# Kernel tuning notes

Measured on AMD Instinct MI355X. Metric: run time of the kernel, lower is better.

## Reference

```python
import jax, jax.numpy as jnp
import numpy as np

P = 31998
VOCAB = P + 2        # 32000
EMBED = 1024
HIDDEN = 2048
NUM_LAYERS = 4
BATCH = 64
SEQ = 512


def setup_inputs() -> dict:
    key = jax.random.key(0)
    ks = jax.random.split(key, 7)
    X = jax.random.randint(ks[0], (BATCH, SEQ), 0, VOCAB, dtype=jnp.int64 if jax.config.jax_enable_x64 else jnp.int32)
    emb = jax.random.normal(ks[1], (VOCAB, EMBED), dtype=jnp.float32)
    W_xh = jax.random.normal(ks[2], (EMBED, HIDDEN), dtype=jnp.float32)
    W_hh = jax.random.normal(ks[3], (HIDDEN, HIDDEN), dtype=jnp.float32)
    W_hy = jax.random.normal(ks[4], (HIDDEN, VOCAB), dtype=jnp.float32)
    b_h = jnp.zeros((HIDDEN,), dtype=jnp.float32)
    b_y = jnp.zeros((VOCAB,), dtype=jnp.float32)
    return {"X": X, "emb": emb, "W_xh": W_xh, "W_hh": W_hh, "W_hy": W_hy, "b_h": b_h, "b_y": b_y}


def reference(X, emb, W_xh, W_hh, W_hy, b_h, b_y):
    # Original torch code re-initializes new_h from x_t each timestep (no state
    # carried across t), so every timestep is independent and only the last
    # timestep feeds the output. Vectorize over all timesteps faithfully.
    x = emb[X]                                   # [B, T, E]
    h = jnp.tanh(jnp.einsum('bte,eh->bth', x, W_xh) + b_h)   # [B, T, H]
    for _ in range(NUM_LAYERS):
        h = jnp.tanh(jnp.einsum('bth,hk->btk', h, W_hh) + b_h)
    out = h[:, -1, :] @ W_hy + b_y               # [B, VOCAB]  (last timestep only)
    return out
```

## Files before the change

### kernel.cpp

```cpp
#include <hip/hip_runtime.h>
#include <hip/hip_bf16.h>

#define BATCH 64
#define SEQT  512
#define EMB   1024
#define HID   2048
#define VOC   32000
#define KSPLIT 8

using bf16x8 = __attribute__((ext_vector_type(8))) __bf16;
using f32x4  = __attribute__((ext_vector_type(4))) float;

__device__ __forceinline__ void split2(float x, __bf16& hi, __bf16& lo) {
  hi = (__bf16)x;
  lo = (__bf16)(x - (float)hi);
}

template <int KTOT, bool GATHER, bool PACKOUT>
__global__ __launch_bounds__(1024) void layer_kernel(
    const int* __restrict__ X, const float* __restrict__ emb,
    const __hip_bfloat16* __restrict__ hin_hi,
    const __hip_bfloat16* __restrict__ hin_lo,
    const float* __restrict__ W, const float* __restrict__ bias,
    __hip_bfloat16* __restrict__ hout_hi,
    __hip_bfloat16* __restrict__ hout_lo,
    unsigned* __restrict__ hp, float* __restrict__ hf) {
  constexpr int KCHUNK = KTOT / 16;
  constexpr int KSTEPS = KCHUNK / 32;
  __shared__ float red[16 * 16 * 40];

  const int tid = threadIdx.x;
  const int w = tid >> 6;
  const int l = tid & 63;
  const int ln = l & 15;
  const int lg = l >> 4;
  const int n0 = (blockIdx.x & 127) * 16;
  const int mb = (blockIdx.x >> 7) * 32;

  f32x4 acc[2];
#pragma unroll
  for (int mt = 0; mt < 2; ++mt) acc[mt] = f32x4{0.f, 0.f, 0.f, 0.f};

  const float* grow[2];
#pragma unroll
  for (int mt = 0; mt < 2; ++mt) {
    if constexpr (GATHER) {
      const int m = mb + ln + 16 * mt;
      const int tok = X[m * SEQT + (SEQT - 1)];
      grow[mt] = emb + (size_t)tok * EMB;
    } else {
      grow[mt] = nullptr;
    }
  }

  const int kwave = w * KCHUNK + lg * 8;
  const float* Wc = W + n0 + ln;

  float wv[KSTEPS * 8];
#pragma unroll
  for (int j = 0; j < KSTEPS * 8; ++j)
    wv[j] = Wc[(size_t)(kwave + (j >> 3) * 32 + (j & 7)) * HID];

  bf16x8 Ah[2][KSTEPS], Al[2][KSTEPS];
  if constexpr (GATHER) {
#pragma unroll
    for (int mt = 0; mt < 2; ++mt)
#pragma unroll
      for (int ks = 0; ks < KSTEPS; ++ks) {
        const float* p = grow[mt] + kwave + ks * 32;
        const f32x4 v0 = *reinterpret_cast<const f32x4*>(p);
        const f32x4 v1 = *reinterpret_cast<const f32x4*>(p + 4);
#pragma unroll
        for (int i = 0; i < 4; ++i) {
          __bf16 h_, l_;
          split2(v0[i], h_, l_);
          Ah[mt][ks][i] = h_;
          Al[mt][ks][i] = l_;
          split2(v1[i], h_, l_);
          Ah[mt][ks][4 + i] = h_;
          Al[mt][ks][4 + i] = l_;
        }
      }
  } else {
#pragma unroll
    for (int mt = 0; mt < 2; ++mt)
#pragma unroll
      for (int ks = 0; ks < KSTEPS; ++ks) {
        const size_t off = (size_t)(mb + ln + 16 * mt) * KTOT + kwave + ks * 32;
        Ah[mt][ks] = *reinterpret_cast<const bf16x8*>(hin_hi + off);
        Al[mt][ks] = *reinterpret_cast<const bf16x8*>(hin_lo + off);
      }
  }

#pragma unroll
  for (int ks = 0; ks < KSTEPS; ++ks) {
    bf16x8 bhi, blo;
#pragma unroll
    for (int i = 0; i < 8; ++i) {
      __bf16 h_, l_;
      split2(wv[ks * 8 + i], h_, l_);
      bhi[i] = h_;
      blo[i] = l_;
    }
#pragma unroll
    for (int mt = 0; mt < 2; ++mt) {
      acc[mt] = __builtin_amdgcn_mfma_f32_16x16x32_bf16(Ah[mt][ks], bhi, acc[mt], 0, 0, 0);
      acc[mt] = __builtin_amdgcn_mfma_f32_16x16x32_bf16(Al[mt][ks], bhi, acc[mt], 0, 0, 0);
      acc[mt] = __builtin_amdgcn_mfma_f32_16x16x32_bf16(Ah[mt][ks], blo, acc[mt], 0, 0, 0);
    }
  }

  float* dst = &red[(w * 16 + ln) * 40 + lg * 4];
#pragma unroll
  for (int mt = 0; mt < 2; ++mt)
    *reinterpret_cast<f32x4*>(dst + mt * 16) = acc[mt];

  __syncthreads();

  if (tid < 512) {
    const int m = tid >> 4, n = tid & 15;
    float s = 0.f;
#pragma unroll
    for (int ww = 0; ww < 16; ++ww) s += red[(ww * 16 + n) * 40 + m];
    s += bias[n0 + n];
    const float hval = tanhf(s);
    if constexpr (PACKOUT) {
      const int c = n0 + n;
      const int mg = mb + m;
      hf[(size_t)c * 64 + mg] = hval;
      const float partner = __shfl_xor(hval, 1, 64);
      if ((tid & 1) == 0) {
        using fp2 = __attribute__((ext_vector_type(2))) __fp16;
        const fp2 pk = __builtin_amdgcn_cvt_pkrtz(hval, partner);
        hp[(size_t)(c >> 1) * 64 + mg] = __builtin_bit_cast(unsigned, pk);
      }
    } else {
      __bf16 h_, l_;
      split2(hval, h_, l_);
      const size_t off = (size_t)(mb + m) * HID + (n0 + n);
      hout_hi[off] = *reinterpret_cast<__hip_bfloat16*>(&h_);
      hout_lo[off] = *reinterpret_cast<__hip_bfloat16*>(&l_);
    }
  }
}

__global__ __launch_bounds__(256) void out_mfma(
    const __hip_bfloat16* __restrict__ hhi, const float* __restrict__ Why,
    float* __restrict__ scratch) {
  __shared__ float lds[2 * 32 * 128];

  const int tid = threadIdx.x;
  const int w = tid >> 6;
  const int l = tid & 63;
  const int ln = l & 15;
  const int lg = l >> 4;
  const int nt = blockIdx.x % 250;
  const int kq = blockIdx.x / 250;
  const int n0 = nt * 128;
  const int k0 = kq * 256;

  const int srow = tid >> 5;
  const int scol = (tid & 31) * 4;

  f32x4 acc[4][2];
#pragma unroll
  for (int mf = 0; mf < 4; ++mf)
#pragma unroll
    for (int nf = 0; nf < 2; ++nf) acc[mf][nf] = f32x4{0.f, 0.f, 0.f, 0.f};

  f32x4 st[4];

#define GLOAD(ks_)                                                           \
  {                                                                          \
    _Pragma("unroll") for (int i = 0; i < 4; ++i) {                          \
      st[i] = __builtin_nontemporal_load(reinterpret_cast<const f32x4*>(     \
          Why + (size_t)(k0 + (ks_) * 32 + srow + i * 8) * VOC + n0 + scol));\
    }                                                                        \
  }

#define DSWRITE(buf_)                                                        \
  {                                                                          \
    float* lb_ = lds + (buf_) * (32 * 128);                                  \
    _Pragma("unroll") for (int i = 0; i < 4; ++i) {                          \
      *reinterpret_cast<f32x4*>(lb_ + (srow + i * 8) * 128 + scol) = st[i];  \
    }                                                                        \
  }

#define COMPUTE(buf_, ks_)                                                   \
  {                                                                          \
    const float* lb_ = lds + (buf_) * (32 * 128);                            \
    bf16x8 a_[4];                                                            \
    _Pragma("unroll") for (int mf = 0; mf < 4; ++mf) {                       \
      a_[mf] = *reinterpret_cast<const bf16x8*>(                             \
          hhi + (size_t)(mf * 16 + ln) * HID + k0 + (ks_) * 32 + lg * 8);    \
    }                                                                        \
    bf16x8 b_[2];                                                            \
    _Pragma("unroll") for (int nf = 0; nf < 2; ++nf) {                       \
      _Pragma("unroll") for (int i = 0; i < 8; ++i) {                        \
        b_[nf][i] =                                                          \
            (__bf16)lb_[(lg * 8 + i) * 128 + w * 32 + nf * 16 + ln];         \
      }                                                                      \
    }                                                                        \
    _Pragma("unroll") for (int mf = 0; mf < 4; ++mf) {                       \
      _Pragma("unroll") for (int nf = 0; nf < 2; ++nf) {                     \
        acc[mf][nf] = __builtin_amdgcn_mfma_f32_16x16x32_bf16(               \
            a_[mf], b_[nf], acc[mf][nf], 0, 0, 0);                           \
      }                                                                      \
    }                                                                        \
  }

  GLOAD(0);
  DSWRITE(0);
  __syncthreads();

#pragma unroll
  for (int ks = 0; ks < 8; ++ks) {
    if (ks < 7) GLOAD(ks + 1);
    COMPUTE(ks & 1, ks);
    __syncthreads();
    if (ks < 7) {
      DSWRITE((ks + 1) & 1);
      __syncthreads();
    }
  }
#undef COMPUTE
#undef DSWRITE
#undef GLOAD

  float* sc = scratch + (size_t)kq * ((size_t)BATCH * VOC);
#pragma unroll
  for (int mf = 0; mf < 4; ++mf) {
#pragma unroll
    for (int nf = 0; nf < 2; ++nf) {
#pragma unroll
      for (int j = 0; j < 4; ++j) {
        const int row = mf * 16 + lg * 4 + j;
        const int col = n0 + w * 32 + nf * 16 + ln;
        sc[(size_t)row * VOC + col] = acc[mf][nf][j];
      }
    }
  }
}

__global__ __launch_bounds__(256) void reduce_out(
    const float* __restrict__ scratch, const float* __restrict__ by,
    float* __restrict__ out) {
  const int n = blockIdx.x * 256 + threadIdx.x;
  const int m = blockIdx.y;
  float s = by[n];
#pragma unroll
  for (int q = 0; q < KSPLIT; ++q)
    s += scratch[(size_t)q * ((size_t)BATCH * VOC) + (size_t)m * VOC + n];
  __builtin_nontemporal_store(s, out + (size_t)m * VOC + n);
}

extern "C" void kernel_launch(void* const* d_in, const int* in_sizes, int n_in,
                              void* d_out, int out_size, void* d_ws,
                              size_t ws_size, hipStream_t stream) {
  const int* X = (const int*)d_in[0];
  const float* emb = (const float*)d_in[1];
  const float* W_xh = (const float*)d_in[2];
  const float* W_hh = (const float*)d_in[3];
  const float* W_hy = (const float*)d_in[4];
  const float* b_h = (const float*)d_in[5];
  const float* b_y = (const float*)d_in[6];
  float* out = (float*)d_out;

  char* ws = (char*)d_ws;
  const size_t PLANE = (size_t)BATCH * HID;
  __hip_bfloat16* hA_hi = (__hip_bfloat16*)ws;
  __hip_bfloat16* hA_lo = hA_hi + PLANE;
  __hip_bfloat16* hB_hi = hA_lo + PLANE;
  __hip_bfloat16* hB_lo = hB_hi + PLANE;
  float* scratch = (float*)(ws + 4 * PLANE * sizeof(__hip_bfloat16));

  dim3 blk(1024), grd(256);
  layer_kernel<EMB, true, false><<<grd, blk, 0, stream>>>(
      X, emb, nullptr, nullptr, W_xh, b_h, hA_hi, hA_lo, nullptr, nullptr);
  layer_kernel<HID, false, false><<<grd, blk, 0, stream>>>(
      nullptr, nullptr, hA_hi, hA_lo, W_hh, b_h, hB_hi, hB_lo, nullptr, nullptr);
  layer_kernel<HID, false, false><<<grd, blk, 0, stream>>>(
      nullptr, nullptr, hB_hi, hB_lo, W_hh, b_h, hA_hi, hA_lo, nullptr, nullptr);
  layer_kernel<HID, false, false><<<grd, blk, 0, stream>>>(
      nullptr, nullptr, hA_hi, hA_lo, W_hh, b_h, hB_hi, hB_lo, nullptr, nullptr);
  layer_kernel<HID, false, false><<<grd, blk, 0, stream>>>(
      nullptr, nullptr, hB_hi, hB_lo, W_hh, b_h, hA_hi, hA_lo, nullptr, nullptr);

  out_mfma<<<dim3(2000), dim3(256), 0, stream>>>(hA_hi, W_hy, scratch);
  reduce_out<<<dim3(125, 64), dim3(256), 0, stream>>>(scratch, b_y, out);
}
```

Before: 136.6 us.

## Halve output GEMM k-split and use triple-buffered LDS pipeline with single barrier

The output projection now splits K into 4 chunks of 512 instead of 8 of 256, so 1000 blocks each run 16 k-steps and the reduce kernel sums fewer partial planes. The LDS staging moves from double to triple buffering with two register staging sets, which lets global loads run two steps ahead and drops one __syncthreads per step. The unused PACKOUT path is removed from the layer kernel. The trade-offs are fewer blocks in flight, more LDS and register use per block, and a longer serial loop per block.

Measured after the change: 126.3 us. 7.5% less time.

```diff
diff --git a/kernel.cpp b/kernel.cpp
--- a/kernel.cpp
+++ b/kernel.cpp
@@ -6,7 +6,7 @@
 #define EMB   1024
 #define HID   2048
 #define VOC   32000
-#define KSPLIT 8
+#define KSPLIT 4
 
 using bf16x8 = __attribute__((ext_vector_type(8))) __bf16;
 using f32x4  = __attribute__((ext_vector_type(4))) float;
@@ -16,15 +16,14 @@
   lo = (__bf16)(x - (float)hi);
 }
 
-template <int KTOT, bool GATHER, bool PACKOUT>
+template <int KTOT, bool GATHER>
 __global__ __launch_bounds__(1024) void layer_kernel(
     const int* __restrict__ X, const float* __restrict__ emb,
     const __hip_bfloat16* __restrict__ hin_hi,
     const __hip_bfloat16* __restrict__ hin_lo,
     const float* __restrict__ W, const float* __restrict__ bias,
     __hip_bfloat16* __restrict__ hout_hi,
-    __hip_bfloat16* __restrict__ hout_lo,
-    unsigned* __restrict__ hp, float* __restrict__ hf) {
+    __hip_bfloat16* __restrict__ hout_lo) {
   constexpr int KCHUNK = KTOT / 16;
   constexpr int KSTEPS = KCHUNK / 32;
   __shared__ float red[16 * 16 * 40];
@@ -124,30 +123,18 @@
     for (int ww = 0; ww < 16; ++ww) s += red[(ww * 16 + n) * 40 + m];
     s += bias[n0 + n];
     const float hval = tanhf(s);
-    if constexpr (PACKOUT) {
-      const int c = n0 + n;
-      const int mg = mb + m;
-      hf[(size_t)c * 64 + mg] = hval;
-      const float partner = __shfl_xor(hval, 1, 64);
-      if ((tid & 1) == 0) {
-        using fp2 = __attribute__((ext_vector_type(2))) __fp16;
-        const fp2 pk = __builtin_amdgcn_cvt_pkrtz(hval, partner);
-        hp[(size_t)(c >> 1) * 64 + mg] = __builtin_bit_cast(unsigned, pk);
-      }
-    } else {
-      __bf16 h_, l_;
-      split2(hval, h_, l_);
-      const size_t off = (size_t)(mb + m) * HID + (n0 + n);
-      hout_hi[off] = *reinterpret_cast<__hip_bfloat16*>(&h_);
-      hout_lo[off] = *reinterpret_cast<__hip_bfloat16*>(&l_);
-    }
+    __bf16 h_, l_;
+    split2(hval, h_, l_);
+    const size_t off = (size_t)(mb + m) * HID + (n0 + n);
+    hout_hi[off] = *reinterpret_cast<__hip_bfloat16*>(&h_);
+    hout_lo[off] = *reinterpret_cast<__hip_bfloat16*>(&l_);
   }
 }
 
 __global__ __launch_bounds__(256) void out_mfma(
     const __hip_bfloat16* __restrict__ hhi, const float* __restrict__ Why,
     float* __restrict__ scratch) {
-  __shared__ float lds[2 * 32 * 128];
+  __shared__ float lds[3 * 32 * 128];
 
   const int tid = threadIdx.x;
   const int w = tid >> 6;
@@ -157,7 +144,8 @@
   const int nt = blockIdx.x % 250;
   const int kq = blockIdx.x / 250;
   const int n0 = nt * 128;
-  const int k0 = kq * 256;
+  const int k0 = kq * 512;
+  constexpr int NS = 16;
 
   const int srow = tid >> 5;
   const int scol = (tid & 31) * 4;
@@ -168,21 +156,21 @@
 #pragma unroll
     for (int nf = 0; nf < 2; ++nf) acc[mf][nf] = f32x4{0.f, 0.f, 0.f, 0.f};
 
-  f32x4 st[4];
-
-#define GLOAD(ks_)                                                           \
+  f32x4 stA[4], stB[4];
+
+#define GLOAD(ks_, st_)                                                      \
   {                                                                          \
     _Pragma("unroll") for (int i = 0; i < 4; ++i) {                          \
-      st[i] = __builtin_nontemporal_load(reinterpret_cast<const f32x4*>(     \
+      st_[i] = __builtin_nontemporal_load(reinterpret_cast<const f32x4*>(    \
           Why + (size_t)(k0 + (ks_) * 32 + srow + i * 8) * VOC + n0 + scol));\
     }                                                                        \
   }
 
-#define DSWRITE(buf_)                                                        \
+#define DSWRITE(buf_, st_)                                                   \
   {                                                                          \
     float* lb_ = lds + (buf_) * (32 * 128);                                  \
     _Pragma("unroll") for (int i = 0; i < 4; ++i) {                          \
-      *reinterpret_cast<f32x4*>(lb_ + (srow + i * 8) * 128 + scol) = st[i];  \
+      *reinterpret_cast<f32x4*>(lb_ + (srow + i * 8) * 128 + scol) = st_[i]; \
     }                                                                        \
   }
 
@@ -209,19 +197,22 @@
     }                                                                        \
   }
 
-  GLOAD(0);
-  DSWRITE(0);
+  GLOAD(0, stA);
+  DSWRITE(0, stA);
+  GLOAD(1, stB);
   __syncthreads();
 
 #pragma unroll
-  for (int ks = 0; ks < 8; ++ks) {
-    if (ks < 7) GLOAD(ks + 1);
-    COMPUTE(ks & 1, ks);
-    __syncthreads();
-    if (ks < 7) {
-      DSWRITE((ks + 1) & 1);
-      __syncthreads();
-    }
+  for (int ks = 0; ks < NS; ++ks) {
+    if (ks + 2 < NS) {
+      if ((ks & 1) == 0) GLOAD(ks + 2, stA) else GLOAD(ks + 2, stB);
+    }
+    if (ks + 1 < NS) {
+      if (((ks + 1) & 1) == 0) DSWRITE((ks + 1) % 3, stA)
+      else DSWRITE((ks + 1) % 3, stB);
+    }
+    COMPUTE(ks % 3, ks);
+    if (ks + 1 < NS) __syncthreads();
   }
 #undef COMPUTE
 #undef DSWRITE
@@ -275,17 +266,17 @@
   float* scratch = (float*)(ws + 4 * PLANE * sizeof(__hip_bfloat16));
 
   dim3 blk(1024), grd(256);
-  layer_kernel<EMB, true, false><<<grd, blk, 0, stream>>>(
-      X, emb, nullptr, nullptr, W_xh, b_h, hA_hi, hA_lo, nullptr, nullptr);
-  layer_kernel<HID, false, false><<<grd, blk, 0, stream>>>(
-      nullptr, nullptr, hA_hi, hA_lo, W_hh, b_h, hB_hi, hB_lo, nullptr, nullptr);
-  layer_kernel<HID, false, false><<<grd, blk, 0, stream>>>(
-      nullptr, nullptr, hB_hi, hB_lo, W_hh, b_h, hA_hi, hA_lo, nullptr, nullptr);
-  layer_kernel<HID, false, false><<<grd, blk, 0, stream>>>(
-      nullptr, nullptr, hA_hi, hA_lo, W_hh, b_h, hB_hi, hB_lo, nullptr, nullptr);
-  layer_kernel<HID, false, false><<<grd, blk, 0, stream>>>(
-      nullptr, nullptr, hB_hi, hB_lo, W_hh, b_h, hA_hi, hA_lo, nullptr, nullptr);
-
-  out_mfma<<<dim3(2000), dim3(256), 0, stream>>>(hA_hi, W_hy, scratch);
+  layer_kernel<EMB, true><<<grd, blk, 0, stream>>>(
+      X, emb, nullptr, nullptr, W_xh, b_h, hA_hi, hA_lo);
+  layer_kernel<HID, false><<<grd, blk, 0, stream>>>(
+      nullptr, nullptr, hA_hi, hA_lo, W_hh, b_h, hB_hi, hB_lo);
+  layer_kernel<HID, false><<<grd, blk, 0, stream>>>(
+      nullptr, nullptr, hB_hi, hB_lo, W_hh, b_h, hA_hi, hA_lo);
+  layer_kernel<HID, false><<<grd, blk, 0, stream>>>(
+      nullptr, nullptr, hA_hi, hA_lo, W_hh, b_h, hB_hi, hB_lo);
+  layer_kernel<HID, false><<<grd, blk, 0, stream>>>(
+      nullptr, nullptr, hB_hi, hB_lo, W_hh, b_h, hA_hi, hA_lo);
+
+  out_mfma<<<dim3(1000), dim3(256), 0, stream>>>(hA_hi, W_hy, scratch);
   reduce_out<<<dim3(125, 64), dim3(256), 0, stream>>>(scratch, b_y, out);
 }
```
